# Kernel optimization log

Measured on AMD Instinct MI355X. Metric: run time of the kernel, lower is better.

## Reference

```python
import jax, jax.numpy as jnp
import numpy as np

B, NP, DL, DA, H, NB = 8, 81920, 16, 4, 128, 3
DT_TOTAL = DL + DA  # 20
NSTEPS = 4
DT = 0.1


def setup_inputs() -> dict:
    key = jax.random.key(0)
    k1, k2, k3, k4 = jax.random.split(key, 4)
    inputs = jax.random.normal(k1, (B, NP, DT_TOTAL), dtype=jnp.float32)
    neighbours = jax.random.randint(k2, (NP, NB), 0, NP, dtype=jnp.int64)
    fan_in = NB * DT_TOTAL  # 60
    W1 = jax.random.normal(k3, (fan_in, H), dtype=jnp.float32) / np.sqrt(fan_in)
    b1 = jnp.zeros((H,), dtype=jnp.float32)
    W2 = jax.random.normal(k4, (H, DL), dtype=jnp.float32) / np.sqrt(H)
    b2 = jnp.zeros((DL,), dtype=jnp.float32)
    return {"inputs": inputs, "neighbours": neighbours, "W1": W1, "b1": b1, "W2": W2, "b2": b2}


def reference(inputs, neighbours, W1, b1, W2, b2):
    """nsteps of forward Euler: Y[..., :DL] += dt * Phi(gather(Y, neighbours))."""
    Y = inputs
    for _ in range(NSTEPS):
        # neighbour gather: (B, NP, NB, DT_TOTAL)
        Z = Y[:, neighbours, :]
        # shared interaction MLP on flattened neighbourhood features
        Zf = Z.reshape(B, NP, NB * DT_TOTAL)
        h = jnp.tanh(jnp.einsum('bpf,fh->bph', Zf, W1) + b1)
        fZ = jnp.einsum('bph,hd->bpd', h, W2) + b2  # (B, NP, DL)
        # pad with zeros over ancillary dims == update only latent slice
        Y = Y.at[..., :DL].add(DT * fZ)
    return Y
```

## Files before the change

### kernel.cpp

```cpp
#include <hip/hip_runtime.h>

#define B_DIM   8
#define NPTS    81920
#define DTOT    20
#define DT_STEP 0.1f

#define BLOCK 64
#define GRID  5120
#define ITERS 8
#define NFRAG 21
#define FIMG_BYTES 32768
#define TANH_SCALE 2.885390082f

#define MDL_ROW 32
#define MDA_ROW 8

typedef __attribute__((ext_vector_type(8))) short    short8;
typedef __attribute__((ext_vector_type(4))) float    f32x4;
typedef __attribute__((ext_vector_type(2))) unsigned u32x2;
typedef __attribute__((ext_vector_type(4))) unsigned u32x4;
typedef __attribute__((ext_vector_type(2))) short    short2v;

__device__ __forceinline__ unsigned short f2bf(float f) {
    unsigned u = __builtin_bit_cast(unsigned, f);
    u += 0x7FFFu + ((u >> 16) & 1u);
    return (unsigned short)(u >> 16);
}
#if __has_builtin(__builtin_amdgcn_cvt_pk_bf16_f32)
__device__ __forceinline__ unsigned pack2(float a, float b) {
    short2v p = __builtin_amdgcn_cvt_pk_bf16_f32(a, b);
    return __builtin_bit_cast(unsigned, p);
}
#else
__device__ __forceinline__ unsigned pack2(float a, float b) {
    return (unsigned)f2bf(a) | ((unsigned)f2bf(b) << 16);
}
#endif
__device__ __forceinline__ float tanh_folded(float a) {
    float e = __builtin_amdgcn_exp2f(a);
    float r = __builtin_amdgcn_rcpf(1.0f + e);
    return 1.0f - 2.0f * r;
}

__device__ __forceinline__ int feat_of(int ks, int q, int j) {
    if (ks == 0) {
        if (q == 0) return j;
        if (q == 1) return 8 + j;
        if (q == 2) return 20 + j;
        return (j < 4) ? 16 + j : 36 + (j - 4);
    }
    if (q == 0) return 28 + j;
    if (q == 1) return 40 + j;
    if (q == 2) return 48 + j;
    if (j < 4) return 56 + j;
    return (j == 4) ? 60 : 61;
}

__device__ __forceinline__ int hid_of(int ks, int q, int j) {
    return (2 * ks + (j >> 2)) * 16 + q * 4 + (j & 3);
}

__global__ __launch_bounds__(256) void build_mirror(
    const f32x4* __restrict__ in, char* __restrict__ m0dl,
    char* __restrict__ mda, f32x4* __restrict__ outF, int n4,
    const float* __restrict__ W1, const float* __restrict__ b1,
    const float* __restrict__ W2, const float* __restrict__ b2,
    char* __restrict__ img)
{
    const int i = blockIdx.x * 256 + threadIdx.x;
    if (i < n4) {
        f32x4 v = in[i];
        u32x2 o; o.x = pack2(v.x, v.y); o.y = pack2(v.z, v.w);
        const int r = i / 5, c = i % 5;
        if (c < 4) {
            *(u32x2*)(m0dl + (size_t)r * MDL_ROW + c * 8) = o;
        } else {
            *(u32x2*)(mda + (size_t)r * MDA_ROW) = o;
            outF[i] = v;
        }
    }
    if (blockIdx.x == 0) {
        const int t = threadIdx.x, lane = t & 63, g = t >> 6;
        const int l15 = lane & 15, q = lane >> 4;
        for (int f = g; f < NFRAG; f += 4) {
            char* dst = img + (f * 64 + lane) * 16;
            if (f < 16) {
                const int nt = f >> 1, ks = f & 1, m = nt * 16 + l15;
                unsigned short v[8];
                #pragma unroll
                for (int j = 0; j < 8; j++) {
                    const int ft = feat_of(ks, q, j);
                    float x = (ft < 60) ? TANH_SCALE * W1[ft * 128 + m]
                                        : (ft == 60 ? TANH_SCALE * b1[m] : 0.0f);
                    v[j] = f2bf(x);
                }
                *(u32x4*)dst = *(const u32x4*)v;
            } else if (f < 20) {
                const int ks = f - 16;
                unsigned short v[8];
                #pragma unroll
                for (int j = 0; j < 8; j++) {
                    const int H = hid_of(ks, q, j);
                    v[j] = f2bf(DT_STEP * W2[H * 16 + l15]);
                }
                *(u32x4*)dst = *(const u32x4*)v;
            } else {
                f32x4 a = { DT_STEP * b2[q * 4 + 0], DT_STEP * b2[q * 4 + 1],
                            DT_STEP * b2[q * 4 + 2], DT_STEP * b2[q * 4 + 3] };
                *(f32x4*)dst = a;
            }
        }
    }
}

__device__ __forceinline__ void gather3(
    const char* __restrict__ MdlB, const char* __restrict__ MdaB,
    int nx0, int nx1, int nx2,
    int offA, int offB, bool selA, bool selB, bool q3,
    u32x4& A, u32x4& Bv, u32x2& C)
{
    const int rA = selA ? nx1 : nx0;
    const int rB = selB ? nx2 : nx1;
    const char* aA = q3 ? (MdaB + (size_t)nx0 * MDA_ROW)
                        : (MdlB + (size_t)rA * MDL_ROW + offA);
    const char* aB = q3 ? (MdaB + (size_t)nx1 * MDA_ROW)
                        : (MdlB + (size_t)rB * MDL_ROW + offB);
    A  = *(const u32x4*)aA;
    Bv = *(const u32x4*)aB;
    u32x2 c = { 0u, 0u };
    if (q3) c = *(const u32x2*)(MdaB + (size_t)nx2 * MDA_ROW);
    C = c;
}

__global__ __launch_bounds__(BLOCK) void neural_step(
    const float* __restrict__ Yin, float* __restrict__ Yout,
    const char* __restrict__ Mdl_in, char* __restrict__ Mdl_out,
    const char* __restrict__ Mda,
    const int* __restrict__ nbr, const char* __restrict__ img,
    const int inStride, const int outStride, const int writeMirror)
{
    const int t = threadIdx.x, lane = t & 63;
    const int l15 = lane & 15, q = lane >> 4;
    const bool q3 = (q == 3);
    const bool selA = (q == 2);
    const bool selB = (q == 1) || (q == 2);
    const int offA = (q == 1) ? 16 : 0;
    const int offB = (q == 0) || (q == 2) ? 16 : 0;

    const int bk = blockIdx.x;
    const int bB = bk & 7;
    const int p0 = (bk >> 3) * (ITERS * 16) + l15;
    const size_t rowBase = (size_t)bB * NPTS;
    const char* MdlB = Mdl_in  + (size_t)bB * NPTS * MDL_ROW;
    char*       MdoB = Mdl_out + (size_t)bB * NPTS * MDL_ROW;
    const char* MdaB = Mda     + (size_t)bB * NPTS * MDA_ROW;

    int nx0, nx1, nx2, ny0 = 0, ny1 = 0, ny2 = 0;
    u32x4 gA, gB, nA = {0,0,0,0}, nB = {0,0,0,0};
    u32x2 gC, nC = {0,0};
    f32x4 ownC, ownN = {0.f, 0.f, 0.f, 0.f};
    {
        const int* np = nbr + (size_t)p0 * 3;
        nx0 = np[0]; nx1 = np[1]; nx2 = np[2];
        gather3(MdlB, MdaB, nx0, nx1, nx2, offA, offB, selA, selB, q3,
                gA, gB, gC);
        ownC = __builtin_nontemporal_load(
            (const f32x4*)(Yin + (rowBase + p0) * inStride) + q);
        const int* np1 = nbr + (size_t)(p0 + 16) * 3;
        nx0 = np1[0]; nx1 = np1[1]; nx2 = np1[2];
    }

    const short8* frg = (const short8*)img;
    short8 B1f[8][2];
    #pragma unroll
    for (int nt = 0; nt < 8; nt++)
        #pragma unroll
        for (int ks = 0; ks < 2; ks++)
            B1f[nt][ks] = frg[(nt * 2 + ks) * 64 + lane];
    short8 W2f[4];
    #pragma unroll
    for (int ks = 0; ks < 4; ks++)
        W2f[ks] = frg[(16 + ks) * 64 + lane];
    const f32x4 acc2init = ((const f32x4*)img)[20 * 64 + lane];

    #pragma unroll
    for (int it = 0; it < ITERS; it++) {
        if (it + 1 < ITERS) {
            ownN = __builtin_nontemporal_load(
                (const f32x4*)(Yin + (rowBase + p0 + (it + 1) * 16) * inStride) + q);
            gather3(MdlB, MdaB, nx0, nx1, nx2, offA, offB, selA, selB, q3,
                    nA, nB, nC);
        }
        if (it + 2 < ITERS) {
            const int* np = nbr + (size_t)(p0 + (it + 2) * 16) * 3;
            ny0 = np[0]; ny1 = np[1]; ny2 = np[2];
        }

        u32x4 u0 = { gA.x, gA.y, q3 ? gB.x : gA.z, q3 ? gB.y : gA.w };
        u32x4 u1 = { q3 ? gC.x : gB.x, q3 ? gC.y : gB.y,
                     q3 ? 0x00003F80u : gB.z, q3 ? 0u : gB.w };
        short8 zb0 = __builtin_bit_cast(short8, u0);
        short8 zb1 = __builtin_bit_cast(short8, u1);

        unsigned hx[8], hy[8];
        #pragma unroll
        for (int nt = 0; nt < 8; nt++) {
            f32x4 acc = { 0.f, 0.f, 0.f, 0.f };
            acc = __builtin_amdgcn_mfma_f32_16x16x32_bf16(B1f[nt][0], zb0, acc, 0, 0, 0);
            acc = __builtin_amdgcn_mfma_f32_16x16x32_bf16(B1f[nt][1], zb1, acc, 0, 0, 0);
            hx[nt] = pack2(tanh_folded(acc[0]), tanh_folded(acc[1]));
            hy[nt] = pack2(tanh_folded(acc[2]), tanh_folded(acc[3]));
        }

        f32x4 acc2 = acc2init;
        #pragma unroll
        for (int ks = 0; ks < 4; ks++) {
            u32x4 hu = { hx[2 * ks], hy[2 * ks], hx[2 * ks + 1], hy[2 * ks + 1] };
            acc2 = __builtin_amdgcn_mfma_f32_16x16x32_bf16(
                W2f[ks], __builtin_bit_cast(short8, hu), acc2, 0, 0, 0);
        }

        const size_t row = rowBase + (size_t)(p0 + it * 16);
        f32x4 o = ownC;
        o.x += acc2[0]; o.y += acc2[1]; o.z += acc2[2]; o.w += acc2[3];
        *((f32x4*)(Yout + row * outStride) + q) = o;
        if (writeMirror) {
            char* mrow = MdoB + (size_t)(p0 + it * 16) * MDL_ROW;
            u32x2 mw; mw.x = pack2(o.x, o.y); mw.y = pack2(o.z, o.w);
            *(u32x2*)(mrow + q * 8) = mw;
        }

        ownC = ownN;
        gA = nA; gB = nB; gC = nC;
        nx0 = ny0; nx1 = ny1; nx2 = ny2;
    }
}

extern "C" void kernel_launch(void* const* d_in, const int* in_sizes, int n_in,
                              void* d_out, int out_size, void* d_ws, size_t ws_size,
                              hipStream_t stream) {
    const float* inputs = (const float*)d_in[0];
    const int*   nbr    = (const int*)  d_in[1];
    const float* W1     = (const float*)d_in[2];
    const float* b1     = (const float*)d_in[3];
    const float* W2     = (const float*)d_in[4];
    const float* b2     = (const float*)d_in[5];
    float* out = (float*)d_out;

    const size_t MDL_BYTES = (size_t)B_DIM * NPTS * MDL_ROW;
    const size_t MDA_BYTES = (size_t)B_DIM * NPTS * MDA_ROW;
    const size_t PBYTES    = (size_t)B_DIM * NPTS * 16 * 4;
    char* M0 = (char*)d_ws;
    char* M1 = (char*)d_ws + MDL_BYTES;
    char* DA = (char*)d_ws + 2 * MDL_BYTES;
    char* FI = DA + MDA_BYTES;
    float* P = (float*)(FI + FIMG_BYTES);

    const bool usePacked =
        ws_size >= 2 * MDL_BYTES + MDA_BYTES + FIMG_BYTES + PBYTES;
    float* mid  = usePacked ? P : out;
    const int sMid = usePacked ? 16 : DTOT;

    const int n4 = B_DIM * NPTS * DTOT / 4;
    build_mirror<<<n4 / 256, 256, 0, stream>>>(
        (const f32x4*)inputs, M0, DA, (f32x4*)out, n4,
        W1, b1, W2, b2, FI);

    const dim3 grid(GRID), block(BLOCK);
    neural_step<<<grid, block, 0, stream>>>(inputs, mid, M0, M1, DA, nbr, FI,
                                            DTOT, sMid, 1);
    neural_step<<<grid, block, 0, stream>>>(mid, mid, M1, M0, DA, nbr, FI,
                                            sMid, sMid, 1);
    neural_step<<<grid, block, 0, stream>>>(mid, mid, M0, M1, DA, nbr, FI,
                                            sMid, sMid, 1);
    neural_step<<<grid, block, 0, stream>>>(mid, out, M1, M0, DA, nbr, FI,
                                            sMid, DTOT, 0);
}
```

Baseline: 291.7 us.

## Carry latent state in bf16 mirror between steps instead of fp32 buffer

Each Euler step now reads its own latent state from the bf16 mirror rather than an fp32 intermediate array. Intermediate steps write only the bf16 mirror, and only the last step writes fp32 output with a nontemporal store. This removes the fp32 read and write traffic per intermediate step. In exchange, the state is rounded to bf16 at every step, so accumulated error across the Euler steps grows compared with the fp32 residual path.

```diff
diff --git a/kernel.cpp b/kernel.cpp
--- a/kernel.cpp
+++ b/kernel.cpp
@@ -36,6 +36,14 @@
     return (unsigned)f2bf(a) | ((unsigned)f2bf(b) << 16);
 }
 #endif
+__device__ __forceinline__ f32x4 unpack4(u32x2 m) {
+    f32x4 o;
+    o.x = __builtin_bit_cast(float, m.x << 16);
+    o.y = __builtin_bit_cast(float, m.x & 0xffff0000u);
+    o.z = __builtin_bit_cast(float, m.y << 16);
+    o.w = __builtin_bit_cast(float, m.y & 0xffff0000u);
+    return o;
+}
 __device__ __forceinline__ float tanh_folded(float a) {
     float e = __builtin_amdgcn_exp2f(a);
     float r = __builtin_amdgcn_rcpf(1.0f + e);
@@ -133,11 +141,11 @@
 }
 
 __global__ __launch_bounds__(BLOCK) void neural_step(
-    const float* __restrict__ Yin, float* __restrict__ Yout,
+    float* __restrict__ Yout,
     const char* __restrict__ Mdl_in, char* __restrict__ Mdl_out,
     const char* __restrict__ Mda,
     const int* __restrict__ nbr, const char* __restrict__ img,
-    const int inStride, const int outStride, const int writeMirror)
+    const int last)
 {
     const int t = threadIdx.x, lane = t & 63;
     const int l15 = lane & 15, q = lane >> 4;
@@ -158,14 +166,13 @@
     int nx0, nx1, nx2, ny0 = 0, ny1 = 0, ny2 = 0;
     u32x4 gA, gB, nA = {0,0,0,0}, nB = {0,0,0,0};
     u32x2 gC, nC = {0,0};
-    f32x4 ownC, ownN = {0.f, 0.f, 0.f, 0.f};
+    u32x2 ownC, ownN = {0u, 0u};
     {
         const int* np = nbr + (size_t)p0 * 3;
         nx0 = np[0]; nx1 = np[1]; nx2 = np[2];
         gather3(MdlB, MdaB, nx0, nx1, nx2, offA, offB, selA, selB, q3,
                 gA, gB, gC);
-        ownC = __builtin_nontemporal_load(
-            (const f32x4*)(Yin + (rowBase + p0) * inStride) + q);
+        ownC = *(const u32x2*)(MdlB + (size_t)p0 * MDL_ROW + q * 8);
         const int* np1 = nbr + (size_t)(p0 + 16) * 3;
         nx0 = np1[0]; nx1 = np1[1]; nx2 = np1[2];
     }
@@ -186,8 +193,8 @@
     #pragma unroll
     for (int it = 0; it < ITERS; it++) {
         if (it + 1 < ITERS) {
-            ownN = __builtin_nontemporal_load(
-                (const f32x4*)(Yin + (rowBase + p0 + (it + 1) * 16) * inStride) + q);
+            ownN = *(const u32x2*)(MdlB + (size_t)(p0 + (it + 1) * 16) * MDL_ROW
+                                   + q * 8);
             gather3(MdlB, MdaB, nx0, nx1, nx2, offA, offB, selA, selB, q3,
                     nA, nB, nC);
         }
@@ -220,14 +227,15 @@
                 W2f[ks], __builtin_bit_cast(short8, hu), acc2, 0, 0, 0);
         }
 
-        const size_t row = rowBase + (size_t)(p0 + it * 16);
-        f32x4 o = ownC;
+        f32x4 o = unpack4(ownC);
         o.x += acc2[0]; o.y += acc2[1]; o.z += acc2[2]; o.w += acc2[3];
-        *((f32x4*)(Yout + row * outStride) + q) = o;
-        if (writeMirror) {
+        if (!last) {
             char* mrow = MdoB + (size_t)(p0 + it * 16) * MDL_ROW;
             u32x2 mw; mw.x = pack2(o.x, o.y); mw.y = pack2(o.z, o.w);
             *(u32x2*)(mrow + q * 8) = mw;
+        } else {
+            const size_t row = rowBase + (size_t)(p0 + it * 16);
+            __builtin_nontemporal_store(o, (f32x4*)(Yout + row * DTOT) + q);
         }
 
         ownC = ownN;
@@ -249,17 +257,10 @@
 
     const size_t MDL_BYTES = (size_t)B_DIM * NPTS * MDL_ROW;
     const size_t MDA_BYTES = (size_t)B_DIM * NPTS * MDA_ROW;
-    const size_t PBYTES    = (size_t)B_DIM * NPTS * 16 * 4;
     char* M0 = (char*)d_ws;
     char* M1 = (char*)d_ws + MDL_BYTES;
     char* DA = (char*)d_ws + 2 * MDL_BYTES;
     char* FI = DA + MDA_BYTES;
-    float* P = (float*)(FI + FIMG_BYTES);
-
-    const bool usePacked =
-        ws_size >= 2 * MDL_BYTES + MDA_BYTES + FIMG_BYTES + PBYTES;
-    float* mid  = usePacked ? P : out;
-    const int sMid = usePacked ? 16 : DTOT;
 
     const int n4 = B_DIM * NPTS * DTOT / 4;
     build_mirror<<<n4 / 256, 256, 0, stream>>>(
@@ -267,12 +268,8 @@
         W1, b1, W2, b2, FI);
 
     const dim3 grid(GRID), block(BLOCK);
-    neural_step<<<grid, block, 0, stream>>>(inputs, mid, M0, M1, DA, nbr, FI,
-                                            DTOT, sMid, 1);
-    neural_step<<<grid, block, 0, stream>>>(mid, mid, M1, M0, DA, nbr, FI,
-                                            sMid, sMid, 1);
-    neural_step<<<grid, block, 0, stream>>>(mid, mid, M0, M1, DA, nbr, FI,
-                                            sMid, sMid, 1);
-    neural_step<<<grid, block, 0, stream>>>(mid, out, M1, M0, DA, nbr, FI,
-                                            sMid, DTOT, 0);
-}
+    neural_step<<<grid, block, 0, stream>>>(out, M0, M1, DA, nbr, FI, 0);
+    neural_step<<<grid, block, 0, stream>>>(out, M1, M0, DA, nbr, FI, 0);
+    neural_step<<<grid, block, 0, stream>>>(out, M0, M1, DA, nbr, FI, 0);
+    neural_step<<<grid, block, 0, stream>>>(out, M1, M0, DA, nbr, FI, 1);
+}
```

Measured after the change: 265.4 us. -9.0%, faster.
